# Optimization experiments

Hardware: AMD Instinct MI355X
Metric: run time of the kernel (lower is better)

## Reference

```python
import jax, jax.numpy as jnp
import numpy as np

# Mamba-1.4B-like dims
BATCH, SEQ, HID = 1, 2048, 2048
INTER, STATE, DT_RANK, KCONV = 4096, 16, 128, 4


def setup_inputs() -> dict:
    key = jax.random.key(0)
    ks = jax.random.split(key, 8)
    f = jnp.float32
    return {
        "input_states": jax.random.normal(ks[0], (BATCH, SEQ, HID), f),
        "in_proj_w": jax.random.normal(ks[1], (HID, 2 * INTER), f) * (HID ** -0.5),
        "conv_w": jax.random.normal(ks[2], (INTER, 1, KCONV), f) * (KCONV ** -0.5),  # (O, I/groups=1, K) depthwise
        "conv_b": jnp.zeros((INTER,), f),
        "x_proj_w": jax.random.normal(ks[3], (INTER, DT_RANK + 2 * STATE), f) * (INTER ** -0.5),
        "dt_proj_w": jax.random.normal(ks[4], (DT_RANK, INTER), f) * (DT_RANK ** -0.5),
        "dt_proj_b": jax.random.normal(ks[5], (INTER,), f) * 0.1,
        "A_log": jnp.log(jnp.broadcast_to(jnp.arange(1, STATE + 1, dtype=f), (INTER, STATE))),
        "D": jnp.ones((INTER,), f),
        "out_proj_w": jax.random.normal(ks[6], (INTER, HID), f) * (INTER ** -0.5),
    }


def _mamba_forward(input_states, in_proj_w, conv_w, conv_b, x_proj_w,
                   dt_proj_w, dt_proj_b, A_log, D, out_proj_w):
    Bsz, L, _ = input_states.shape
    Idim, _, K = conv_w.shape
    N = A_log.shape[1]
    R = dt_proj_w.shape[0]

    proj = input_states @ in_proj_w                       # (B, L, 2I)
    hidden, gate = jnp.split(proj, 2, axis=-1)            # each (B, L, I)

    # depthwise causal conv over sequence (pad K-1, keep first L outputs)
    xc = jnp.swapaxes(hidden, 1, 2)                       # (B, I, L)
    xc = jax.lax.conv_general_dilated(
        xc, conv_w, window_strides=(1,), padding=((K - 1, K - 1),),
        feature_group_count=Idim)
    xc = xc[:, :, :L] + conv_b[None, :, None]
    u = jax.nn.silu(jnp.swapaxes(xc, 1, 2))               # (B, L, I)

    # input-dependent SSM params
    ssm_in = u @ x_proj_w                                 # (B, L, R + 2N)
    dt_in, Bc, Cc = jnp.split(ssm_in, [R, R + N], axis=-1)
    dt = jax.nn.softplus(dt_in @ dt_proj_w + dt_proj_b)   # (B, L, I)
    A = -jnp.exp(A_log)                                   # (I, N)

    def step(state, xs):
        dt_t, B_t, C_t, u_t = xs                          # (B,I) (B,N) (B,N) (B,I)
        dA = jnp.exp(dt_t[:, :, None] * A[None])          # (B, I, N)
        state = state * dA + (dt_t * u_t)[:, :, None] * B_t[:, None, :]
        y_t = jnp.einsum('bin,bn->bi', state, C_t)
        return state, y_t

    xs = (jnp.swapaxes(dt, 0, 1), jnp.swapaxes(Bc, 0, 1),
          jnp.swapaxes(Cc, 0, 1), jnp.swapaxes(u, 0, 1))
    state0 = jnp.zeros((Bsz, Idim, N), dt.dtype)
    _, ys = jax.lax.scan(step, state0, xs)                # (L, B, I)
    y = jnp.swapaxes(ys, 0, 1)                            # (B, L, I)

    y = (y + u * D) * jax.nn.silu(gate)
    return y @ out_proj_w                                 # (B, L, H)


def reference(input_states, in_proj_w, conv_w, conv_b, x_proj_w,
              dt_proj_w, dt_proj_b, A_log, D, out_proj_w):
    return _mamba_forward(input_states, in_proj_w, conv_w, conv_b, x_proj_w,
                          dt_proj_w, dt_proj_b, A_log, D, out_proj_w)
```

## Files before the change

### kernel.cpp

```cpp
#include <hip/hip_runtime.h>
#include <stdint.h>

#define LSEQ 2048
#define HID  2048
#define IDIM 4096
#define NSTATE 16
#define RRANK 128
#define GDIM 160

#define GCHUNK 64
#define TCHUNK (LSEQ / GCHUNK)

typedef _Float16 f16x8 __attribute__((ext_vector_type(8)));
typedef float f32x4 __attribute__((ext_vector_type(4)));

#define GLOAD_LDS16(g, l) __builtin_amdgcn_global_load_lds( \
    (const __attribute__((address_space(1))) void*)(g),     \
    (__attribute__((address_space(3))) void*)(l), 16, 0, 0)

__global__ void f32_to_f16_kernel(const float* __restrict__ in, _Float16* __restrict__ out, int n) {
    int i = blockIdx.x * 256 + threadIdx.x;
    if (i < n) out[i] = (_Float16)in[i];
}

__global__ void transpose_f32_f16_kernel(const float* __restrict__ in, _Float16* __restrict__ out,
                                         int R, int C) {
    __shared__ float tile[32][33];
    int bx = blockIdx.x;
    int by = blockIdx.y;
    int tx = threadIdx.x & 31;
    int ty = threadIdx.x >> 5;
    int r0 = by * 32, c0 = bx * 32;
    #pragma unroll
    for (int j = 0; j < 32; j += 8)
        tile[ty + j][tx] = in[(long)(r0 + ty + j) * C + c0 + tx];
    __syncthreads();
    #pragma unroll
    for (int j = 0; j < 32; j += 8)
        out[(long)(c0 + ty + j) * R + r0 + tx] = (_Float16)tile[tx][ty + j];
}

#define BM 128
#define BK 32

template <typename CT, int BN_>
__global__ __launch_bounds__(256)
void gemm_bt_kernel(const _Float16* __restrict__ A, const _Float16* __restrict__ Bt,
                    CT* __restrict__ C, int M, int N, int K, int kc) {
    constexpr int NI = BN_ / 32;
    __shared__ _Float16 As[BM * BK];
    __shared__ _Float16 Bs[BN_ * BK];
    const int m0 = blockIdx.y * BM;
    const int n0 = blockIdx.x * BN_;
    const int t = threadIdx.x;
    const int wave = t >> 6;
    const int lane = t & 63;
    const int wm = wave >> 1, wn = wave & 1;
    const int lrow = lane & 15;
    const int quad = lane >> 4;
    const int qoff = (quad * 8) ^ (((lrow >> 1) & 3) * 8);

    f32x4 acc[4][NI];
    #pragma unroll
    for (int mi = 0; mi < 4; ++mi)
        #pragma unroll
        for (int ni = 0; ni < NI; ++ni)
            #pragma unroll
            for (int r = 0; r < 4; ++r)
                acc[mi][ni][r] = 0.f;

    int ra[2], ca[2];
    #pragma unroll
    for (int j = 0; j < 2; ++j) {
        int p = wave * 128 + j * 64 + lane;
        ra[j] = p >> 2;
        ca[j] = ((p & 3) ^ ((ra[j] >> 1) & 3)) * 8;
    }
    int rb[BN_ / 64], cb_[BN_ / 64];
    #pragma unroll
    for (int j = 0; j < BN_ / 64; ++j) {
        int p = wave * BN_ + j * 64 + lane;
        rb[j] = p >> 2;
        cb_[j] = ((p & 3) ^ ((rb[j] >> 1) & 3)) * 8;
    }

    const int k_begin = blockIdx.z * kc;
    const int k_end = k_begin + kc;

    for (int kk = k_begin; kk < k_end; kk += BK) {
        #pragma unroll
        for (int j = 0; j < 2; ++j)
            GLOAD_LDS16(A + (long)(m0 + ra[j]) * K + kk + ca[j],
                        As + (wave * 128 + j * 64) * 8);
        #pragma unroll
        for (int j = 0; j < BN_ / 64; ++j)
            GLOAD_LDS16(Bt + (long)(n0 + rb[j]) * K + kk + cb_[j],
                        Bs + (wave * BN_ + j * 64) * 8);
        __syncthreads();

        f16x8 af[4], bf[NI];
        #pragma unroll
        for (int mi = 0; mi < 4; ++mi)
            af[mi] = *(const f16x8*)(As + (wm * 64 + mi * 16 + lrow) * BK + qoff);
        #pragma unroll
        for (int ni = 0; ni < NI; ++ni)
            bf[ni] = *(const f16x8*)(Bs + (wn * (BN_ / 2) + ni * 16 + lrow) * BK + qoff);
        #pragma unroll
        for (int mi = 0; mi < 4; ++mi)
            #pragma unroll
            for (int ni = 0; ni < NI; ++ni)
                acc[mi][ni] = __builtin_amdgcn_mfma_f32_16x16x32_f16(af[mi], bf[ni], acc[mi][ni], 0, 0, 0);
        __syncthreads();
    }

    CT* Cz = C + (long)blockIdx.z * M * N;
    #pragma unroll
    for (int mi = 0; mi < 4; ++mi) {
        #pragma unroll
        for (int ni = 0; ni < NI; ++ni) {
            int col = n0 + wn * (BN_ / 2) + ni * 16 + lrow;
            if (col < N) {
                #pragma unroll
                for (int r = 0; r < 4; ++r) {
                    int row = m0 + wm * 64 + mi * 16 + quad * 4 + r;
                    Cz[(long)row * N + col] = (CT)acc[mi][ni][r];
                }
            }
        }
    }
}

__global__ void xproj_reduce_kernel(const float* __restrict__ part, float* __restrict__ ssm,
                                    _Float16* __restrict__ dtin) {
    int idx = blockIdx.x * 256 + threadIdx.x;
    if (idx >= LSEQ * GDIM) return;
    int t = idx / GDIM;
    int c = idx - t * GDIM;
    float v = 0.f;
    #pragma unroll
    for (int k = 0; k < 8; ++k)
        v += part[((long)k * LSEQ + t) * 256 + c];
    ssm[idx] = v;
    if (c < RRANK) dtin[t * RRANK + c] = (_Float16)v;
}

__global__ void conv_silu_kernel(const _Float16* __restrict__ proj, const float* __restrict__ w,
                                 const float* __restrict__ b, _Float16* __restrict__ u16) {
    int idx = blockIdx.x * 256 + threadIdx.x;
    int i0 = (idx & 511) * 8;
    int t = idx >> 9;
    const long rowbase = (long)t * (2 * IDIM) + i0;
    f16x8 x0, xm1 = {0,0,0,0,0,0,0,0}, xm2 = {0,0,0,0,0,0,0,0}, xm3 = {0,0,0,0,0,0,0,0};
    x0 = *(const f16x8*)(proj + rowbase);
    if (t >= 1) xm1 = *(const f16x8*)(proj + rowbase - 1 * 2 * IDIM);
    if (t >= 2) xm2 = *(const f16x8*)(proj + rowbase - 2 * 2 * IDIM);
    if (t >= 3) xm3 = *(const f16x8*)(proj + rowbase - 3 * 2 * IDIM);
    f16x8 res;
    #pragma unroll
    for (int j = 0; j < 8; ++j) {
        float4 wv = ((const float4*)w)[i0 + j];
        float a = b[i0 + j]
                + (float)xm3[j] * wv.x + (float)xm2[j] * wv.y
                + (float)xm1[j] * wv.z + (float)x0[j] * wv.w;
        res[j] = (_Float16)(a / (1.f + __expf(-a)));
    }
    *(f16x8*)(u16 + (long)t * IDIM + i0) = res;
}

__device__ __forceinline__ float softplus_f(float x) {
    if (x > 20.f) return x;
    return log1pf(__expf(x));
}
__device__ __forceinline__ float silu_f(float x) {
    return x / (1.f + __expf(-x));
}

__global__ __launch_bounds__(256)
void scan_pass1_kernel(const float* __restrict__ dtlin, const float* __restrict__ dtb,
                       const float* __restrict__ ssm, const _Float16* __restrict__ u16,
                       const float* __restrict__ A_log,
                       float* __restrict__ Pc, float* __restrict__ Sc) {
    const int c = blockIdx.y;
    const int i = blockIdx.x * 256 + threadIdx.x;

    __shared__ float Bs[TCHUNK * 16];
    for (int idx = threadIdx.x; idx < TCHUNK * 16; idx += 256) {
        int t = idx >> 4, n = idx & 15;
        Bs[idx] = ssm[(c * TCHUNK + t) * GDIM + RRANK + n];
    }
    __syncthreads();

    float A[16];
    {
        const float4* Ap = (const float4*)(A_log + i * 16);
        #pragma unroll
        for (int q = 0; q < 4; ++q) {
            float4 v = Ap[q];
            A[q * 4 + 0] = -__expf(v.x);
            A[q * 4 + 1] = -__expf(v.y);
            A[q * 4 + 2] = -__expf(v.z);
            A[q * 4 + 3] = -__expf(v.w);
        }
    }
    const float dtbi = dtb[i];

    float s[16], p[16];
    #pragma unroll
    for (int n = 0; n < 16; ++n) { s[n] = 0.f; p[n] = 1.f; }

    long base = (long)c * TCHUNK * IDIM + i;
    for (int t = 0; t < TCHUNK; ++t) {
        float dt = softplus_f(dtlin[base + (long)t * IDIM] + dtbi);
        float dtu = dt * (float)u16[base + (long)t * IDIM];
        #pragma unroll
        for (int n = 0; n < 16; ++n) {
            float dA = __expf(dt * A[n]);
            s[n] = s[n] * dA + dtu * Bs[t * 16 + n];
            p[n] *= dA;
        }
    }

    long o = ((long)c * IDIM + i) * 16;
    #pragma unroll
    for (int q = 0; q < 4; ++q) {
        *(float4*)(Pc + o + q * 4) = make_float4(p[q*4+0], p[q*4+1], p[q*4+2], p[q*4+3]);
        *(float4*)(Sc + o + q * 4) = make_float4(s[q*4+0], s[q*4+1], s[q*4+2], s[q*4+3]);
    }
}

__global__ void scan_combine_kernel(const float* __restrict__ Pc, float* __restrict__ ScInit) {
    int tid = blockIdx.x * 256 + threadIdx.x;
    float carry = 0.f;
    for (int c = 0; c < GCHUNK; ++c) {
        long o = (long)c * (IDIM * 16) + tid;
        float pv = Pc[o];
        float sv = ScInit[o];
        ScInit[o] = carry;
        carry = carry * pv + sv;
    }
}

__global__ __launch_bounds__(256)
void scan_pass3_kernel(const float* __restrict__ dtlin, const float* __restrict__ dtb,
                       const float* __restrict__ ssm, const _Float16* __restrict__ u16,
                       const _Float16* __restrict__ proj, const float* __restrict__ A_log,
                       const float* __restrict__ Dp, const float* __restrict__ Init,
                       _Float16* __restrict__ y16) {
    const int c = blockIdx.y;
    const int i = blockIdx.x * 256 + threadIdx.x;

    __shared__ float Bs[TCHUNK * 16];
    __shared__ float Cs[TCHUNK * 16];
    for (int idx = threadIdx.x; idx < TCHUNK * 16; idx += 256) {
        int t = idx >> 4, n = idx & 15;
        Bs[idx] = ssm[(c * TCHUNK + t) * GDIM + RRANK + n];
        Cs[idx] = ssm[(c * TCHUNK + t) * GDIM + RRANK + NSTATE + n];
    }
    __syncthreads();

    float A[16];
    {
        const float4* Ap = (const float4*)(A_log + i * 16);
        #pragma unroll
        for (int q = 0; q < 4; ++q) {
            float4 v = Ap[q];
            A[q * 4 + 0] = -__expf(v.x);
            A[q * 4 + 1] = -__expf(v.y);
            A[q * 4 + 2] = -__expf(v.z);
            A[q * 4 + 3] = -__expf(v.w);
        }
    }
    const float dtbi = dtb[i];
    const float Dv = Dp[i];

    float s[16];
    {
        long o = ((long)c * IDIM + i) * 16;
        #pragma unroll
        for (int q = 0; q < 4; ++q) {
            float4 v = *(const float4*)(Init + o + q * 4);
            s[q*4+0] = v.x; s[q*4+1] = v.y; s[q*4+2] = v.z; s[q*4+3] = v.w;
        }
    }

    long base = (long)c * TCHUNK * IDIM + i;
    for (int t = 0; t < TCHUNK; ++t) {
        float dt = softplus_f(dtlin[base + (long)t * IDIM] + dtbi);
        float uv = (float)u16[base + (long)t * IDIM];
        float dtu = dt * uv;
        float y = 0.f;
        #pragma unroll
        for (int n = 0; n < 16; ++n) {
            float dA = __expf(dt * A[n]);
            s[n] = s[n] * dA + dtu * Bs[t * 16 + n];
            y += s[n] * Cs[t * 16 + n];
        }
        int tg = c * TCHUNK + t;
        float g = (float)proj[(long)tg * (2 * IDIM) + IDIM + i];
        float out = (y + uv * Dv) * silu_f(g);
        y16[base + (long)t * IDIM] = (_Float16)out;
    }
}

extern "C" void kernel_launch(void* const* d_in, const int* in_sizes, int n_in,
                              void* d_out, int out_size, void* d_ws, size_t ws_size,
                              hipStream_t stream) {
    const float* x_in  = (const float*)d_in[0];
    const float* w_in  = (const float*)d_in[1];
    const float* cw    = (const float*)d_in[2];
    const float* cb    = (const float*)d_in[3];
    const float* xw    = (const float*)d_in[4];
    const float* dtw   = (const float*)d_in[5];
    const float* dtb   = (const float*)d_in[6];
    const float* alog  = (const float*)d_in[7];
    const float* Dp    = (const float*)d_in[8];
    const float* ow    = (const float*)d_in[9];
    float* out = (float*)d_out;

    char* p = (char*)d_ws;
    auto alloc = [&](size_t bytes) { char* r = p; p += (bytes + 255) & ~255ull; return r; };
    _Float16* Xf    = (_Float16*)alloc((size_t)LSEQ * HID * 2);
    _Float16* Wt1   = (_Float16*)alloc((size_t)2 * IDIM * HID * 2);
    _Float16* proj  = (_Float16*)alloc((size_t)LSEQ * 2 * IDIM * 2);
    _Float16* u16   = (_Float16*)alloc((size_t)LSEQ * IDIM * 2);
    _Float16* Wt2   = (_Float16*)alloc((size_t)256 * IDIM * 2);
    float*    ssm   = (float*)alloc((size_t)LSEQ * GDIM * 4);
    _Float16* dtin  = (_Float16*)alloc((size_t)LSEQ * RRANK * 2);
    _Float16* Wt3   = (_Float16*)alloc((size_t)IDIM * RRANK * 2);
    float*    dtlin = (float*)alloc((size_t)LSEQ * IDIM * 4);
    _Float16* Wt4   = (_Float16*)alloc((size_t)HID * IDIM * 2);
    _Float16* y16   = (_Float16*)alloc((size_t)LSEQ * IDIM * 2);

    float* xpart = (float*)Wt1;
    float* Pc = (float*)Wt1;
    float* Sc = Pc + (size_t)GCHUNK * IDIM * 16;

    f32_to_f16_kernel<<<(LSEQ * HID) / 256, 256, 0, stream>>>(x_in, Xf, LSEQ * HID);
    transpose_f32_f16_kernel<<<dim3(2 * IDIM / 32, HID / 32), 256, 0, stream>>>(w_in, Wt1, HID, 2 * IDIM);
    transpose_f32_f16_kernel<<<dim3(GDIM / 32, IDIM / 32), 256, 0, stream>>>(xw, Wt2, IDIM, GDIM);
    transpose_f32_f16_kernel<<<dim3(IDIM / 32, RRANK / 32), 256, 0, stream>>>(dtw, Wt3, RRANK, IDIM);
    transpose_f32_f16_kernel<<<dim3(HID / 32, IDIM / 32), 256, 0, stream>>>(ow, Wt4, IDIM, HID);

    gemm_bt_kernel<_Float16, 128><<<dim3(2 * IDIM / 128, LSEQ / BM, 1), 256, 0, stream>>>(
        Xf, Wt1, proj, LSEQ, 2 * IDIM, HID, HID);
    conv_silu_kernel<<<(LSEQ * IDIM / 8) / 256, 256, 0, stream>>>(proj, cw, cb, u16);
    gemm_bt_kernel<float, 128><<<dim3(2, LSEQ / BM, 8), 256, 0, stream>>>(
        u16, Wt2, xpart, LSEQ, 256, IDIM, IDIM / 8);
    xproj_reduce_kernel<<<(LSEQ * GDIM + 255) / 256, 256, 0, stream>>>(xpart, ssm, dtin);
    gemm_bt_kernel<float, 128><<<dim3(IDIM / 128, LSEQ / BM, 1), 256, 0, stream>>>(
        dtin, Wt3, dtlin, LSEQ, IDIM, RRANK, RRANK);
    scan_pass1_kernel<<<dim3(IDIM / 256, GCHUNK), 256, 0, stream>>>(
        dtlin, dtb, ssm, u16, alog, Pc, Sc);
    scan_combine_kernel<<<(IDIM * NSTATE) / 256, 256, 0, stream>>>(Pc, Sc);
    scan_pass3_kernel<<<dim3(IDIM / 256, GCHUNK), 256, 0, stream>>>(
        dtlin, dtb, ssm, u16, proj, alog, Dp, Sc, y16);
    gemm_bt_kernel<float, 64><<<dim3(HID / 64, LSEQ / BM, 1), 256, 0, stream>>>(
        y16, Wt4, out, LSEQ, HID, IDIM, IDIM);
}
```

Before: 552.6 us.

## Deepen GEMM K tile, batch conv timesteps, store dt in fp16, prefetch combine

Raises the GEMM K tile from 32 to 64 with a new 8-chunk XOR swizzle for LDS loads. This halves the number of barrier pairs per K loop. The conv+SiLU kernel now computes four timesteps per thread and reuses the overlapping input rows. The dt projection output is stored as fp16 instead of fp32 to halve scan read traffic, at some precision risk before softplus. The chunk-combine kernel also prefetches four chunks ahead to hide load latency.

```diff
diff --git a/kernel.cpp b/kernel.cpp
--- a/kernel.cpp
+++ b/kernel.cpp
@@ -41,13 +41,14 @@
 }
 
 #define BM 128
-#define BK 32
+#define BK 64
 
 template <typename CT, int BN_>
 __global__ __launch_bounds__(256)
 void gemm_bt_kernel(const _Float16* __restrict__ A, const _Float16* __restrict__ Bt,
                     CT* __restrict__ C, int M, int N, int K, int kc) {
     constexpr int NI = BN_ / 32;
+    constexpr int NISS_B = BN_ * 8 / 256;
     __shared__ _Float16 As[BM * BK];
     __shared__ _Float16 Bs[BN_ * BK];
     const int m0 = blockIdx.y * BM;
@@ -58,7 +59,7 @@
     const int wm = wave >> 1, wn = wave & 1;
     const int lrow = lane & 15;
     const int quad = lane >> 4;
-    const int qoff = (quad * 8) ^ (((lrow >> 1) & 3) * 8);
+    const int sw8 = (lrow & 7) * 8;
 
     f32x4 acc[4][NI];
     #pragma unroll
@@ -69,19 +70,21 @@
             for (int r = 0; r < 4; ++r)
                 acc[mi][ni][r] = 0.f;
 
-    int ra[2], ca[2];
-    #pragma unroll
-    for (int j = 0; j < 2; ++j) {
-        int p = wave * 128 + j * 64 + lane;
-        ra[j] = p >> 2;
-        ca[j] = ((p & 3) ^ ((ra[j] >> 1) & 3)) * 8;
-    }
-    int rb[BN_ / 64], cb_[BN_ / 64];
-    #pragma unroll
-    for (int j = 0; j < BN_ / 64; ++j) {
-        int p = wave * BN_ + j * 64 + lane;
-        rb[j] = p >> 2;
-        cb_[j] = ((p & 3) ^ ((rb[j] >> 1) & 3)) * 8;
+    long gA[4];
+    #pragma unroll
+    for (int j = 0; j < 4; ++j) {
+        int s = j * 256 + t;
+        int row = s >> 3;
+        int ch = (s & 7) ^ (row & 7);
+        gA[j] = (long)(m0 + row) * K + ch * 8;
+    }
+    long gB[NISS_B];
+    #pragma unroll
+    for (int j = 0; j < NISS_B; ++j) {
+        int s = j * 256 + t;
+        int row = s >> 3;
+        int ch = (s & 7) ^ (row & 7);
+        gB[j] = (long)(n0 + row) * K + ch * 8;
     }
 
     const int k_begin = blockIdx.z * kc;
@@ -89,27 +92,29 @@
 
     for (int kk = k_begin; kk < k_end; kk += BK) {
         #pragma unroll
-        for (int j = 0; j < 2; ++j)
-            GLOAD_LDS16(A + (long)(m0 + ra[j]) * K + kk + ca[j],
-                        As + (wave * 128 + j * 64) * 8);
-        #pragma unroll
-        for (int j = 0; j < BN_ / 64; ++j)
-            GLOAD_LDS16(Bt + (long)(n0 + rb[j]) * K + kk + cb_[j],
-                        Bs + (wave * BN_ + j * 64) * 8);
+        for (int j = 0; j < 4; ++j)
+            GLOAD_LDS16(A + gA[j] + kk, As + (j * 256 + wave * 64) * 8);
+        #pragma unroll
+        for (int j = 0; j < NISS_B; ++j)
+            GLOAD_LDS16(Bt + gB[j] + kk, Bs + (j * 256 + wave * 64) * 8);
         __syncthreads();
 
-        f16x8 af[4], bf[NI];
-        #pragma unroll
-        for (int mi = 0; mi < 4; ++mi)
-            af[mi] = *(const f16x8*)(As + (wm * 64 + mi * 16 + lrow) * BK + qoff);
-        #pragma unroll
-        for (int ni = 0; ni < NI; ++ni)
-            bf[ni] = *(const f16x8*)(Bs + (wn * (BN_ / 2) + ni * 16 + lrow) * BK + qoff);
-        #pragma unroll
-        for (int mi = 0; mi < 4; ++mi)
+        #pragma unroll
+        for (int h = 0; h < 2; ++h) {
+            const int qoff = (h * 32 + quad * 8) ^ sw8;
+            f16x8 af[4], bf[NI];
+            #pragma unroll
+            for (int mi = 0; mi < 4; ++mi)
+                af[mi] = *(const f16x8*)(As + (wm * 64 + mi * 16 + lrow) * BK + qoff);
             #pragma unroll
             for (int ni = 0; ni < NI; ++ni)
-                acc[mi][ni] = __builtin_amdgcn_mfma_f32_16x16x32_f16(af[mi], bf[ni], acc[mi][ni], 0, 0, 0);
+                bf[ni] = *(const f16x8*)(Bs + (wn * (BN_ / 2) + ni * 16 + lrow) * BK + qoff);
+            #pragma unroll
+            for (int mi = 0; mi < 4; ++mi)
+                #pragma unroll
+                for (int ni = 0; ni < NI; ++ni)
+                    acc[mi][ni] = __builtin_amdgcn_mfma_f32_16x16x32_f16(af[mi], bf[ni], acc[mi][ni], 0, 0, 0);
+        }
         __syncthreads();
     }
 
@@ -148,23 +153,28 @@
                                  const float* __restrict__ b, _Float16* __restrict__ u16) {
     int idx = blockIdx.x * 256 + threadIdx.x;
     int i0 = (idx & 511) * 8;
-    int t = idx >> 9;
-    const long rowbase = (long)t * (2 * IDIM) + i0;
-    f16x8 x0, xm1 = {0,0,0,0,0,0,0,0}, xm2 = {0,0,0,0,0,0,0,0}, xm3 = {0,0,0,0,0,0,0,0};
-    x0 = *(const f16x8*)(proj + rowbase);
-    if (t >= 1) xm1 = *(const f16x8*)(proj + rowbase - 1 * 2 * IDIM);
-    if (t >= 2) xm2 = *(const f16x8*)(proj + rowbase - 2 * 2 * IDIM);
-    if (t >= 3) xm3 = *(const f16x8*)(proj + rowbase - 3 * 2 * IDIM);
-    f16x8 res;
-    #pragma unroll
-    for (int j = 0; j < 8; ++j) {
-        float4 wv = ((const float4*)w)[i0 + j];
-        float a = b[i0 + j]
-                + (float)xm3[j] * wv.x + (float)xm2[j] * wv.y
-                + (float)xm1[j] * wv.z + (float)x0[j] * wv.w;
-        res[j] = (_Float16)(a / (1.f + __expf(-a)));
-    }
-    *(f16x8*)(u16 + (long)t * IDIM + i0) = res;
+    int t0 = (idx >> 9) * 4;
+    f16x8 r[7];
+    #pragma unroll
+    for (int k = 0; k < 7; ++k) {
+        int tt = t0 - 3 + k;
+        if (tt >= 0) r[k] = *(const f16x8*)(proj + (long)tt * (2 * IDIM) + i0);
+        else         r[k] = f16x8{0,0,0,0,0,0,0,0};
+    }
+    float4 wv[8]; float bb[8];
+    #pragma unroll
+    for (int j = 0; j < 8; ++j) { wv[j] = ((const float4*)w)[i0 + j]; bb[j] = b[i0 + j]; }
+    #pragma unroll
+    for (int tt = 0; tt < 4; ++tt) {
+        f16x8 res;
+        #pragma unroll
+        for (int j = 0; j < 8; ++j) {
+            float a = bb[j] + (float)r[tt][j] * wv[j].x + (float)r[tt+1][j] * wv[j].y
+                            + (float)r[tt+2][j] * wv[j].z + (float)r[tt+3][j] * wv[j].w;
+            res[j] = (_Float16)(a / (1.f + __expf(-a)));
+        }
+        *(f16x8*)(u16 + (long)(t0 + tt) * IDIM + i0) = res;
+    }
 }
 
 __device__ __forceinline__ float softplus_f(float x) {
@@ -176,7 +186,7 @@
 }
 
 __global__ __launch_bounds__(256)
-void scan_pass1_kernel(const float* __restrict__ dtlin, const float* __restrict__ dtb,
+void scan_pass1_kernel(const _Float16* __restrict__ dtlin, const float* __restrict__ dtb,
                        const float* __restrict__ ssm, const _Float16* __restrict__ u16,
                        const float* __restrict__ A_log,
                        float* __restrict__ Pc, float* __restrict__ Sc) {
@@ -210,7 +220,7 @@
 
     long base = (long)c * TCHUNK * IDIM + i;
     for (int t = 0; t < TCHUNK; ++t) {
-        float dt = softplus_f(dtlin[base + (long)t * IDIM] + dtbi);
+        float dt = softplus_f((float)dtlin[base + (long)t * IDIM] + dtbi);
         float dtu = dt * (float)u16[base + (long)t * IDIM];
         #pragma unroll
         for (int n = 0; n < 16; ++n) {
@@ -230,18 +240,37 @@
 
 __global__ void scan_combine_kernel(const float* __restrict__ Pc, float* __restrict__ ScInit) {
     int tid = blockIdx.x * 256 + threadIdx.x;
+    const long stride = (long)IDIM * 16;
+    float p4[4], s4[4];
+    #pragma unroll
+    for (int k = 0; k < 4; ++k) {
+        p4[k] = Pc[(long)k * stride + tid];
+        s4[k] = ScInit[(long)k * stride + tid];
+    }
     float carry = 0.f;
-    for (int c = 0; c < GCHUNK; ++c) {
-        long o = (long)c * (IDIM * 16) + tid;
-        float pv = Pc[o];
-        float sv = ScInit[o];
-        ScInit[o] = carry;
-        carry = carry * pv + sv;
+    for (int g = 0; g < GCHUNK / 4; ++g) {
+        float pc[4], sc[4];
+        #pragma unroll
+        for (int k = 0; k < 4; ++k) { pc[k] = p4[k]; sc[k] = s4[k]; }
+        if (g + 1 < GCHUNK / 4) {
+            #pragma unroll
+            for (int k = 0; k < 4; ++k) {
+                long o2 = (long)((g + 1) * 4 + k) * stride + tid;
+                p4[k] = Pc[o2];
+                s4[k] = ScInit[o2];
+            }
+        }
+        #pragma unroll
+        for (int k = 0; k < 4; ++k) {
+            long o = (long)(g * 4 + k) * stride + tid;
+            ScInit[o] = carry;
+            carry = carry * pc[k] + sc[k];
+        }
     }
 }
 
 __global__ __launch_bounds__(256)
-void scan_pass3_kernel(const float* __restrict__ dtlin, const float* __restrict__ dtb,
+void scan_pass3_kernel(const _Float16* __restrict__ dtlin, const float* __restrict__ dtb,
                        const float* __restrict__ ssm, const _Float16* __restrict__ u16,
                        const _Float16* __restrict__ proj, const float* __restrict__ A_log,
                        const float* __restrict__ Dp, const float* __restrict__ Init,
@@ -285,7 +314,7 @@
 
     long base = (long)c * TCHUNK * IDIM + i;
     for (int t = 0; t < TCHUNK; ++t) {
-        float dt = softplus_f(dtlin[base + (long)t * IDIM] + dtbi);
+        float dt = softplus_f((float)dtlin[base + (long)t * IDIM] + dtbi);
         float uv = (float)u16[base + (long)t * IDIM];
         float dtu = dt * uv;
         float y = 0.f;
@@ -327,7 +356,7 @@
     float*    ssm   = (float*)alloc((size_t)LSEQ * GDIM * 4);
     _Float16* dtin  = (_Float16*)alloc((size_t)LSEQ * RRANK * 2);
     _Float16* Wt3   = (_Float16*)alloc((size_t)IDIM * RRANK * 2);
-    float*    dtlin = (float*)alloc((size_t)LSEQ * IDIM * 4);
+    _Float16* dtlin = (_Float16*)alloc((size_t)LSEQ * IDIM * 2);
     _Float16* Wt4   = (_Float16*)alloc((size_t)HID * IDIM * 2);
     _Float16* y16   = (_Float16*)alloc((size_t)LSEQ * IDIM * 2);
 
@@ -343,11 +372,11 @@
 
     gemm_bt_kernel<_Float16, 128><<<dim3(2 * IDIM / 128, LSEQ / BM, 1), 256, 0, stream>>>(
         Xf, Wt1, proj, LSEQ, 2 * IDIM, HID, HID);
-    conv_silu_kernel<<<(LSEQ * IDIM / 8) / 256, 256, 0, stream>>>(proj, cw, cb, u16);
+    conv_silu_kernel<<<(LSEQ / 4) * (IDIM / 8) / 256, 256, 0, stream>>>(proj, cw, cb, u16);
     gemm_bt_kernel<float, 128><<<dim3(2, LSEQ / BM, 8), 256, 0, stream>>>(
         u16, Wt2, xpart, LSEQ, 256, IDIM, IDIM / 8);
     xproj_reduce_kernel<<<(LSEQ * GDIM + 255) / 256, 256, 0, stream>>>(xpart, ssm, dtin);
-    gemm_bt_kernel<float, 128><<<dim3(IDIM / 128, LSEQ / BM, 1), 256, 0, stream>>>(
+    gemm_bt_kernel<_Float16, 128><<<dim3(IDIM / 128, LSEQ / BM, 1), 256, 0, stream>>>(
         dtin, Wt3, dtlin, LSEQ, IDIM, RRANK, RRANK);
     scan_pass1_kernel<<<dim3(IDIM / 256, GCHUNK), 256, 0, stream>>>(
         dtlin, dtb, ssm, u16, alog, Pc, Sc);
```

Measured after the change: 519.7 us. 6.0% less time.
